# Kernel tuning notes

Measured on AMD Instinct MI355X. Metric: run time of the kernel, lower is better.

The kernel has to match this reference:

```python
import jax, jax.numpy as jnp
import numpy as np

B, C, N, INPUT_DIM = 16, 19, 64, 200
VQ_DIM = 64
NUM_EMBED = 8192
FREQ = INPUT_DIM // 2 + 1  # 101 rfft bins


def setup_inputs() -> dict:
    key = jax.random.key(0)
    k_x, k_pa, k_pp, k_ca, k_cp = jax.random.split(key, 5)
    x = jax.random.normal(k_x, (B, C, N, INPUT_DIM), dtype=jnp.float32)
    # xavier_normal for [FREQ, VQ_DIM]
    std = float(np.sqrt(2.0 / (FREQ + VQ_DIM)))
    proj_amp = jax.random.normal(k_pa, (FREQ, VQ_DIM), dtype=jnp.float32) * std
    proj_phase = jax.random.normal(k_pp, (FREQ, VQ_DIM), dtype=jnp.float32) * std
    codebook_amp = jax.random.uniform(k_ca, (NUM_EMBED, VQ_DIM), dtype=jnp.float32)
    codebook_phase = jax.random.uniform(k_cp, (NUM_EMBED, VQ_DIM), dtype=jnp.float32)
    return {"x": x, "proj_amp": proj_amp, "proj_phase": proj_phase,
            "codebook_amp": codebook_amp, "codebook_phase": codebook_phase}


def _l2norm(v):
    return v / jnp.linalg.norm(v, axis=-1, keepdims=True)


def reference(x, proj_amp, proj_phase, codebook_amp, codebook_phase):
    # rfft over last dim with ortho norm -> [B,C,N,FREQ] complex
    x_fft = jnp.fft.rfft(x, axis=-1, norm="ortho")
    amp = jnp.abs(x_fft)
    phase = jnp.angle(x_fft)
    # project to vq space and L2-normalize features and codebooks
    feat_amp = _l2norm(amp @ proj_amp)        # [B,C,N,D]
    feat_phase = _l2norm(phase @ proj_phase)  # [B,C,N,D]
    cb_amp = _l2norm(codebook_amp)            # [M,D]
    cb_phase = _l2norm(codebook_phase)        # [M,D]
    # cosine similarity vs codebook, argmax over codebook axis
    sim_amp = jnp.einsum("bcnd,md->bcnm", feat_amp, cb_amp)
    sim_phase = jnp.einsum("bcnd,md->bcnm", feat_phase, cb_phase)
    idx_amp = jnp.argmax(sim_amp, axis=-1)
    idx_phase = jnp.argmax(sim_phase, axis=-1)
    return idx_amp, idx_phase
```

## Files before the change

### kernel.cpp

```cpp
#include <hip/hip_runtime.h>
#include <math.h>

constexpr int ROWS  = 19456;
constexpr int IN_DIM = 200;
constexpr int FREQ  = 101;
constexpr int VQD   = 64;
constexpr int NEMB  = 8192;
constexpr int DFT_BLOCKS = ROWS / 8;

typedef __attribute__((ext_vector_type(8))) short short8;
typedef __attribute__((ext_vector_type(4))) float floatx4;

__device__ __forceinline__ unsigned short f2bf(float v) {
    unsigned int u = __builtin_bit_cast(unsigned int, v);
    unsigned int r = u + 0x7fffu + ((u >> 16) & 1u);
    return (unsigned short)(r >> 16);
}
__device__ __forceinline__ float bf2f(unsigned short b) {
    unsigned int u = ((unsigned int)b) << 16;
    return __builtin_bit_cast(float, u);
}

__device__ __forceinline__ void cis_exact(int r, double& c, double& s) {
    if (r == 0)        { c =  1.0; s =  0.0; }
    else if (r == 50)  { c =  0.0; s = -1.0; }
    else if (r == 100) { c = -1.0; s =  0.0; }
    else if (r == 150) { c =  0.0; s =  1.0; }
    else {
        double ang = -6.283185307179586476925286766559 * (double)r / (double)IN_DIM;
        c = cos(ang); s = sin(ang);
    }
}

#define GLOAD_LDS(gp, lp) __builtin_amdgcn_global_load_lds( \
    (const __attribute__((address_space(1))) unsigned int*)(gp), \
    (__attribute__((address_space(3))) unsigned int*)(lp), 16, 0, 0)

constexpr size_t align256(size_t x) { return (x + 255) & ~(size_t)255; }
constexpr size_t SZ_FB    = (size_t)2 * ROWS * VQD * sizeof(unsigned short);
constexpr size_t OFF_FTH  = 0;
constexpr size_t OFF_FTL  = align256(OFF_FTH + SZ_FB);
constexpr size_t SZ_CBB   = (size_t)2 * NEMB * VQD * sizeof(unsigned short);
constexpr size_t OFF_CBH  = align256(OFF_FTL + SZ_FB);
constexpr size_t OFF_CBL  = align256(OFF_CBH + SZ_CBB);
constexpr size_t SZ_FD    = (size_t)2 * ROWS * VQD * sizeof(double);
constexpr size_t OFF_FD   = align256(OFF_CBL + SZ_CBB);
constexpr size_t SZ_INV   = (size_t)2 * NEMB * sizeof(double);
constexpr size_t OFF_INV  = align256(OFF_FD + SZ_FD);
constexpr size_t SZ_PI    = (size_t)2 * 4 * ROWS * sizeof(int);
constexpr size_t OFF_PI1  = align256(OFF_INV + SZ_INV);
constexpr size_t OFF_PI2  = align256(OFF_PI1 + SZ_PI);

__global__ __launch_bounds__(256) void dft_cb_kernel(
    const float* __restrict__ x, const float* __restrict__ projA, const float* __restrict__ projP,
    const float* __restrict__ cbA, const float* __restrict__ cbP,
    unsigned short* __restrict__ ftH, unsigned short* __restrict__ ftL, double* __restrict__ featD,
    unsigned short* __restrict__ cbH, unsigned short* __restrict__ cbL, double* __restrict__ invnD)
{
    __shared__ __align__(16) char smem[20064];
    const int tid = threadIdx.x;

    if (blockIdx.x >= DFT_BLOCKS) {
        float* tile = (float*)smem;
        float* inv  = (float*)(smem + 16640);
        const int bid2 = blockIdx.x - DFT_BLOCKS;
        const int which = bid2 >> 7;
        const int m0 = (bid2 & 127) * 64;
        const float* cb = which ? cbP : cbA;
        for (int e = tid; e < 4096; e += 256) {
            int c = e >> 6, d = e & 63;
            tile[c * 65 + d] = cb[(size_t)(m0 + c) * VQD + d];
        }
        __syncthreads();
        if (tid < 64) {
            double s = 0.0;
            for (int d2 = 0; d2 < 64; ++d2) { double v = (double)tile[tid * 65 + d2]; s += v * v; }
            inv[tid] = (float)(1.0 / sqrt(s));
            invnD[(size_t)which * NEMB + m0 + tid] = 1.0 / sqrt(s);
        }
        __syncthreads();
        for (int e = tid; e < 4096; e += 256) {
            int c = e >> 6, d = e & 63;
            float v = tile[c * 65 + d] * inv[c];
            unsigned short hb = f2bf(v);
            unsigned short lb = f2bf(v - bf2f(hb));
            size_t o = ((size_t)which * NEMB + m0 + c) * VQD + d;
            cbH[o] = hb; cbL[o] = lb;
        }
        return;
    }

    float* xsT  = (float*)smem;
    float* xpS  = (float*)(smem + 7200);
    float* xmS  = (float*)(smem + 10400);
    float* reS  = (float*)(smem + 13600);
    float* imS  = (float*)(smem + 16832);
    float* accS = (float*)(smem + 7200);
    const int r0 = blockIdx.x * 8;

    for (int e = tid; e < 8 * IN_DIM; e += 256) {
        int r = e / IN_DIM, n = e - r * IN_DIM;
        xsT[n * 9 + r] = x[(size_t)(r0 + r) * IN_DIM + n];
    }
    __syncthreads();

    for (int e = tid; e < 99 * 8; e += 256) {
        int n = (e >> 3) + 1, r = e & 7;
        float a = xsT[n * 9 + r];
        float b = xsT[(IN_DIM - n) * 9 + r];
        xpS[n * 8 + r] = a + b;
        xmS[n * 8 + r] = a - b;
    }
    __syncthreads();

    const int k = tid & 127, half = tid >> 7;
    float re[8], im[8];
    if (k < FREQ) {
        double c1, s1;
        cis_exact(k, c1, s1);
        const int n0 = half ? 51 : 1;
        double wc, ws;
        cis_exact((int)(((long long)k * n0) % IN_DIM), wc, ws);
#pragma unroll
        for (int r = 0; r < 8; ++r) { re[r] = 0.f; im[r] = 0.f; }
        if (half) {
            float sg = (k & 1) ? -1.f : 1.f;
#pragma unroll
            for (int r = 0; r < 8; ++r)
                re[r] = xsT[r] + sg * xsT[100 * 9 + r];
        }
        const int nEnd = half ? 100 : 51;
        for (int n = n0; n < nEnd; ++n) {
            const float* xpn = xpS + n * 8;
            const float* xmn = xmS + n * 8;
            float wcf = (float)wc, wsf = (float)ws;
#pragma unroll
            for (int r = 0; r < 8; ++r) {
                re[r] = fmaf(xpn[r], wcf, re[r]);
                im[r] = fmaf(xmn[r], wsf, im[r]);
            }
            double nwc = fma(wc, c1, -ws * s1);
            double nws = fma(wc, s1,  ws * c1);
            wc = nwc; ws = nws;
        }
        if (half) {
#pragma unroll
            for (int r = 0; r < 8; ++r) { reS[k * 8 + r] = re[r]; imS[k * 8 + r] = im[r]; }
        }
    }
    __syncthreads();
    if (half == 0 && k < FREQ) {
#pragma unroll
        for (int r = 0; r < 8; ++r) {
            re[r] += reS[k * 8 + r]; im[r] += imS[k * 8 + r];
            reS[k * 8 + r] = re[r];  imS[k * 8 + r] = im[r];
        }
    }
    __syncthreads();
    for (int e = tid; e < FREQ * 8; e += 256) {
        float c = reS[e], s = imS[e];
        float a2 = fmaf(c, c, s * s);
        float ampv, phv;
        if (a2 >= 0.04f) {
            ampv = sqrtf(a2);
            phv  = atan2f(s, c);
        } else {
            const int kk = e >> 3, rr = e & 7;
            double sg = (kk & 1) ? -1.0 : 1.0;
            double reD = (double)xsT[rr] + sg * (double)xsT[100 * 9 + rr];
            double imD = 0.0;
            double c1, s1;
            cis_exact(kk, c1, s1);
            double wc = c1, ws = s1;
            for (int n = 1; n < 100; ++n) {
                double a = (double)xsT[n * 9 + rr];
                double b = (double)xsT[(IN_DIM - n) * 9 + rr];
                reD = fma(a + b, wc, reD);
                imD = fma(a - b, ws, imD);
                double nwc = fma(wc, c1, -ws * s1);
                double nws = fma(wc, s1,  ws * c1);
                wc = nwc; ws = nws;
            }
            ampv = (float)sqrt(reD * reD + imD * imD);
            phv  = (float)atan2(imD, reD);
        }
        reS[e] = ampv; imS[e] = phv;
    }
    __syncthreads();

    const int d = tid & 63, which = (tid >> 6) & 1, grp = tid >> 7;
    const float* proj = which ? projP : projA;
    const float* srcF = which ? imS : reS;
    float acc[8];
#pragma unroll
    for (int r = 0; r < 8; ++r) acc[r] = 0.f;
    const int kkA = grp ? 51 : 0;
    const int kkB = grp ? FREQ : 51;
    for (int kk = kkA; kk < kkB; ++kk) {
        float p = proj[kk * VQD + d];
#pragma unroll
        for (int r = 0; r < 8; ++r) acc[r] = fmaf(srcF[kk * 8 + r], p, acc[r]);
    }
    if (grp) {
#pragma unroll
        for (int r = 0; r < 8; ++r) accS[(tid & 127) * 8 + r] = acc[r];
    }
    __syncthreads();
    if (grp == 0) {
#pragma unroll
        for (int r = 0; r < 8; ++r) acc[r] += accS[tid * 8 + r];
#pragma unroll
        for (int r = 0; r < 8; ++r) {
            size_t rowi = (size_t)which * ROWS + r0 + r;
            float vf = acc[r];
            unsigned short hb = f2bf(vf);
            unsigned short lb = f2bf(vf - bf2f(hb));
            ftH[rowi * VQD + d] = hb;
            ftL[rowi * VQD + d] = lb;
            featD[rowi * VQD + d] = (double)acc[r];
        }
    }
}

#define MFMA(a, b, c) __builtin_amdgcn_mfma_f32_16x16x32_bf16(a, b, c, 0, 0, 0)
#define UPD(val, s) do { float _v = (val); \
    bool _c1 = _v > b1v[s]; bool _c2 = _v > b2v[s]; \
    b2v[s] = _c1 ? b1v[s] : (_c2 ? _v : b2v[s]); \
    b2i[s] = _c1 ? b1i[s] : (_c2 ? idx : b2i[s]); \
    b1v[s] = _c1 ? _v : b1v[s]; \
    b1i[s] = _c1 ? idx : b1i[s]; } while (0)

__global__ __launch_bounds__(256, 3) void argmax_kernel(
    const unsigned short* __restrict__ ftH, const unsigned short* __restrict__ ftL,
    const unsigned short* __restrict__ cbH, const unsigned short* __restrict__ cbL,
    int* __restrict__ pi1, int* __restrict__ pi2)
{
    __shared__ __align__(16) char lds[33792];
    const int tid = threadIdx.x;
    const int f = blockIdx.y, z = blockIdx.z;
    const int r0 = blockIdx.x * 128;
    const int w = tid >> 6, lane = tid & 63;
    const int q = lane >> 4, cl = lane & 15;

    const unsigned short* ftHb = ftH + (size_t)f * ROWS * VQD;
    const unsigned short* ftLb = ftL + (size_t)f * ROWS * VQD;
    const unsigned short* cbHb = cbH + (size_t)f * NEMB * VQD;
    const unsigned short* cbLb = cbL + (size_t)f * NEMB * VQD;

    short8 aH00, aH01, aH10, aH11, aL00, aL01, aL10, aL11;
    {
        const size_t baseA = (size_t)(r0 + w * 32 + cl) * VQD + q * 8;
        const size_t baseB = baseA + (size_t)16 * VQD;
        aH00 = *(const short8*)(ftHb + baseA);
        aH01 = *(const short8*)(ftHb + baseA + 32);
        aH10 = *(const short8*)(ftHb + baseB);
        aH11 = *(const short8*)(ftHb + baseB + 32);
        aL00 = *(const short8*)(ftLb + baseA);
        aL01 = *(const short8*)(ftLb + baseA + 32);
        aL10 = *(const short8*)(ftLb + baseB);
        aL11 = *(const short8*)(ftLb + baseB + 32);
    }

    float b1v[8], b2v[8]; int b1i[8], b2i[8];
#pragma unroll
    for (int s = 0; s < 8; ++s) { b1v[s] = -INFINITY; b2v[s] = -INFINITY; b1i[s] = 0; b2i[s] = 0; }

    const int cBase = tid >> 3;
    const int jel   = (((tid & 7) ^ (cBase & 7)) << 3);
    const unsigned short* gH = cbHb + (size_t)(z * 2048 + cBase) * VQD + jel;
    const unsigned short* gL = cbLb + (size_t)(z * 2048 + cBase) * VQD + jel;

    const int p0 = ((q ^ (cl & 7)) << 4);
    const int p1 = p0 ^ 64;

#pragma unroll
    for (int r = 0; r < 2; ++r) {
        const size_t gofs = (size_t)(32 * r) * VQD;
        GLOAD_LDS(gH + gofs, lds + w * 1024 + r * 4096);
        GLOAD_LDS(gL + gofs, lds + 8192 + w * 1024 + r * 4096);
    }

    for (int it = 0; it < 32; ++it) {
        __syncthreads();
        if (it < 31) {
            char* nbuf = lds + ((it + 1) & 1) * 16384;
            const size_t gbase = (size_t)((it + 1) * 64) * VQD;
#pragma unroll
            for (int r = 0; r < 2; ++r) {
                const size_t gofs = gbase + (size_t)(32 * r) * VQD;
                GLOAD_LDS(gH + gofs, nbuf + w * 1024 + r * 4096);
                GLOAD_LDS(gL + gofs, nbuf + 8192 + w * 1024 + r * 4096);
            }
        }

        const char* buf = lds + (it & 1) * 16384;
        const int cbase = z * 2048 + it * 64;
#pragma unroll
        for (int nt = 0; nt < 4; ++nt) {
            const char* row = buf + (nt * 16 + cl) * 128;
            short8 bH0 = *(const short8*)(row + p0);
            short8 bH1 = *(const short8*)(row + p1);
            short8 bL0 = *(const short8*)(row + 8192 + p0);
            short8 bL1 = *(const short8*)(row + 8192 + p1);

            floatx4 acc0 = {0.f, 0.f, 0.f, 0.f};
            floatx4 acc1 = {0.f, 0.f, 0.f, 0.f};
            acc0 = MFMA(aH00, bH0, acc0);  acc1 = MFMA(aH10, bH0, acc1);
            acc0 = MFMA(aH01, bH1, acc0);  acc1 = MFMA(aH11, bH1, acc1);
            acc0 = MFMA(aH00, bL0, acc0);  acc1 = MFMA(aH10, bL0, acc1);
            acc0 = MFMA(aH01, bL1, acc0);  acc1 = MFMA(aH11, bL1, acc1);
            acc0 = MFMA(aL00, bH0, acc0);  acc1 = MFMA(aL10, bH0, acc1);
            acc0 = MFMA(aL01, bH1, acc0);  acc1 = MFMA(aL11, bH1, acc1);

            const int idx = cbase + nt * 16 + cl;
#pragma unroll
            for (int i = 0; i < 4; ++i) { UPD(acc0[i], i); UPD(acc1[i], 4 + i); }
        }
    }

    __syncthreads();
    float* redv = (float*)lds;
    int*   redi = (int*)(lds + 128 * 33 * 4);
#pragma unroll
    for (int s = 0; s < 8; ++s) {
        int rowl = w * 32 + ((s & 4) << 2) + q * 4 + (s & 3);
        int base = rowl * 33 + cl * 2;
        redv[base]     = b1v[s]; redi[base]     = b1i[s];
        redv[base + 1] = b2v[s]; redi[base + 1] = b2i[s];
    }
    __syncthreads();
    if (tid < 128) {
        float v1 = -INFINITY, v2 = -INFINITY; int i1 = 0x7fffffff, i2 = 0x7fffffff;
        for (int e = 0; e < 32; ++e) {
            float v = redv[tid * 33 + e]; int id = redi[tid * 33 + e];
            if (v > v1 || (v == v1 && id < i1)) { v2 = v1; i2 = i1; v1 = v; i1 = id; }
            else if (v > v2 || (v == v2 && id < i2)) { v2 = v; i2 = id; }
        }
        size_t p = ((size_t)(f * 4 + z)) * ROWS + r0 + tid;
        pi1[p] = i1; pi2[p] = i2;
    }
}

__global__ __launch_bounds__(256) void rescore_kernel(
    const double* __restrict__ featD, const double* __restrict__ invnD,
    const float* __restrict__ cbA, const float* __restrict__ cbP,
    const int* __restrict__ pi1, const int* __restrict__ pi2,
    int* __restrict__ out)
{
    const int tid = threadIdx.x;
    const int lane = tid & 63, wave = tid >> 6;
    const int task = blockIdx.x * 4 + wave;
    const int f = task / ROWS;
    const int row = task - f * ROWS;
    const float* cb = f ? cbP : cbA;
    const double fd = featD[((size_t)f * ROWS + row) * VQD + lane];

    int idxs[8];
#pragma unroll
    for (int c = 0; c < 8; ++c) {
        int zz = c >> 1;
        size_t p = ((size_t)(f * 4 + zz)) * ROWS + row;
        idxs[c] = (c & 1) ? pi2[p] : pi1[p];
    }
    double cv[8];
#pragma unroll
    for (int c = 0; c < 8; ++c)
        cv[c] = (double)cb[(size_t)idxs[c] * VQD + lane];

    double bestv = -1.0e300; int besti = 0x7fffffff;
#pragma unroll
    for (int c = 0; c < 8; ++c) {
        double t = fd * cv[c];
        for (int m = 32; m >= 1; m >>= 1) t += __shfl_xor(t, m, 64);
        double sim = t * invnD[(size_t)f * NEMB + idxs[c]];
        int idx = idxs[c];
        if (sim > bestv || (sim == bestv && idx < besti)) { bestv = sim; besti = idx; }
    }
    if (lane == 0) out[task] = besti;
}

extern "C" void kernel_launch(void* const* d_in, const int* in_sizes, int n_in,
                              void* d_out, int out_size, void* d_ws, size_t ws_size,
                              hipStream_t stream)
{
    const float* x     = (const float*)d_in[0];
    const float* projA = (const float*)d_in[1];
    const float* projP = (const float*)d_in[2];
    const float* cbA   = (const float*)d_in[3];
    const float* cbP   = (const float*)d_in[4];

    char* ws = (char*)d_ws;
    unsigned short* ftH   = (unsigned short*)(ws + OFF_FTH);
    unsigned short* ftL   = (unsigned short*)(ws + OFF_FTL);
    unsigned short* cbHp  = (unsigned short*)(ws + OFF_CBH);
    unsigned short* cbLp  = (unsigned short*)(ws + OFF_CBL);
    double*         featD = (double*)(ws + OFF_FD);
    double*         invnD = (double*)(ws + OFF_INV);
    int*            pi1   = (int*)(ws + OFF_PI1);
    int*            pi2   = (int*)(ws + OFF_PI2);

    dft_cb_kernel<<<DFT_BLOCKS + 256, 256, 0, stream>>>(
        x, projA, projP, cbA, cbP, ftH, ftL, featD, cbHp, cbLp, invnD);
    argmax_kernel<<<dim3(ROWS / 128, 2, 4), 256, 0, stream>>>(ftH, ftL, cbHp, cbLp, pi1, pi2);
    rescore_kernel<<<(2 * ROWS) / 4, 256, 0, stream>>>(featD, invnD, cbA, cbP, pi1, pi2, (int*)d_out);
}
```

Measured before the change: 306.1 us.

## Share twiddle table in LDS and parallelize rescore over candidates per lane group

The DFT stage now computes the exact cos/sin values once per block into a shared-memory table. The second half's start twiddle is derived from the first-frequency value by a quarter-turn rotation, which replaces two per-thread cis_exact calls. The rescore kernel splits each wave into eight 8-lane groups, one per candidate. Each lane does an 8-element partial dot product, and a shuffle-based argmax reduction follows, replacing eight sequential full-wave reductions. This reduces shuffle count and serial latency, at the cost of an extra barrier and reuse of the reS region for the table.

```diff
diff --git a/kernel.cpp b/kernel.cpp
--- a/kernel.cpp
+++ b/kernel.cpp
@@ -90,12 +90,13 @@
         return;
     }
 
-    float* xsT  = (float*)smem;
-    float* xpS  = (float*)(smem + 7200);
-    float* xmS  = (float*)(smem + 10400);
-    float* reS  = (float*)(smem + 13600);
-    float* imS  = (float*)(smem + 16832);
-    float* accS = (float*)(smem + 7200);
+    float*  xsT  = (float*)smem;
+    float*  xpS  = (float*)(smem + 7200);
+    float*  xmS  = (float*)(smem + 10400);
+    float*  reS  = (float*)(smem + 13600);
+    float*  imS  = (float*)(smem + 16832);
+    double* cisT = (double*)(smem + 13600);
+    float*  accS = (float*)(smem + 7200);
     const int r0 = blockIdx.x * 8;
 
     for (int e = tid; e < 8 * IN_DIM; e += 256) {
@@ -111,16 +112,33 @@
         xpS[n * 8 + r] = a + b;
         xmS[n * 8 + r] = a - b;
     }
+    if (tid < FREQ) {
+        double c, s;
+        cis_exact(tid, c, s);
+        cisT[tid * 2]     = c;
+        cisT[tid * 2 + 1] = s;
+    }
     __syncthreads();
 
     const int k = tid & 127, half = tid >> 7;
+    double c1 = 1.0, s1 = 0.0, wc = 1.0, ws = 0.0;
+    if (k < FREQ) {
+        c1 = cisT[k * 2]; s1 = cisT[k * 2 + 1];
+        if (!half) {
+            wc = c1; ws = s1;
+        } else {
+            switch (k & 3) {
+                case 0: wc =  c1; ws =  s1; break;
+                case 1: wc =  s1; ws = -c1; break;
+                case 2: wc = -c1; ws = -s1; break;
+                default: wc = -s1; ws =  c1; break;
+            }
+        }
+    }
+    __syncthreads();
+
     float re[8], im[8];
     if (k < FREQ) {
-        double c1, s1;
-        cis_exact(k, c1, s1);
-        const int n0 = half ? 51 : 1;
-        double wc, ws;
-        cis_exact((int)(((long long)k * n0) % IN_DIM), wc, ws);
 #pragma unroll
         for (int r = 0; r < 8; ++r) { re[r] = 0.f; im[r] = 0.f; }
         if (half) {
@@ -129,6 +147,7 @@
             for (int r = 0; r < 8; ++r)
                 re[r] = xsT[r] + sg * xsT[100 * 9 + r];
         }
+        const int n0   = half ? 51 : 1;
         const int nEnd = half ? 100 : 51;
         for (int n = n0; n < nEnd; ++n) {
             const float* xpn = xpS + n * 8;
@@ -169,17 +188,17 @@
             double sg = (kk & 1) ? -1.0 : 1.0;
             double reD = (double)xsT[rr] + sg * (double)xsT[100 * 9 + rr];
             double imD = 0.0;
-            double c1, s1;
-            cis_exact(kk, c1, s1);
-            double wc = c1, ws = s1;
+            double cc1, ss1;
+            cis_exact(kk, cc1, ss1);
+            double twc = cc1, tws = ss1;
             for (int n = 1; n < 100; ++n) {
                 double a = (double)xsT[n * 9 + rr];
                 double b = (double)xsT[(IN_DIM - n) * 9 + rr];
-                reD = fma(a + b, wc, reD);
-                imD = fma(a - b, ws, imD);
-                double nwc = fma(wc, c1, -ws * s1);
-                double nws = fma(wc, s1,  ws * c1);
-                wc = nwc; ws = nws;
+                reD = fma(a + b, twc, reD);
+                imD = fma(a - b, tws, imD);
+                double nwc = fma(twc, cc1, -tws * ss1);
+                double nws = fma(twc, ss1,  tws * cc1);
+                twc = nwc; tws = nws;
             }
             ampv = (float)sqrt(reD * reD + imD * imD);
             phv  = (float)atan2(imD, reD);
@@ -353,30 +372,31 @@
     const int f = task / ROWS;
     const int row = task - f * ROWS;
     const float* cb = f ? cbP : cbA;
-    const double fd = featD[((size_t)f * ROWS + row) * VQD + lane];
-
-    int idxs[8];
-#pragma unroll
-    for (int c = 0; c < 8; ++c) {
-        int zz = c >> 1;
-        size_t p = ((size_t)(f * 4 + zz)) * ROWS + row;
-        idxs[c] = (c & 1) ? pi2[p] : pi1[p];
-    }
-    double cv[8];
-#pragma unroll
-    for (int c = 0; c < 8; ++c)
-        cv[c] = (double)cb[(size_t)idxs[c] * VQD + lane];
-
-    double bestv = -1.0e300; int besti = 0x7fffffff;
-#pragma unroll
-    for (int c = 0; c < 8; ++c) {
-        double t = fd * cv[c];
-        for (int m = 32; m >= 1; m >>= 1) t += __shfl_xor(t, m, 64);
-        double sim = t * invnD[(size_t)f * NEMB + idxs[c]];
-        int idx = idxs[c];
-        if (sim > bestv || (sim == bestv && idx < besti)) { bestv = sim; besti = idx; }
-    }
-    if (lane == 0) out[task] = besti;
+
+    const int c  = lane >> 3;
+    const int dp = (lane & 7) * 8;
+
+    const int zz = c >> 1;
+    const size_t p = ((size_t)(f * 4 + zz)) * ROWS + row;
+    const int idx = (c & 1) ? pi2[p] : pi1[p];
+
+    const double* fr = featD + ((size_t)f * ROWS + row) * VQD + dp;
+    const float*  cr = cb + (size_t)idx * VQD + dp;
+    double t = 0.0;
+#pragma unroll
+    for (int j = 0; j < 8; ++j) t = fma(fr[j], (double)cr[j], t);
+    t += __shfl_xor(t, 1, 64);
+    t += __shfl_xor(t, 2, 64);
+    t += __shfl_xor(t, 4, 64);
+    double bv = t * invnD[(size_t)f * NEMB + idx];
+    int    bi = idx;
+#pragma unroll
+    for (int m = 8; m <= 32; m <<= 1) {
+        double ov = __shfl_xor(bv, m, 64);
+        int    oi = __shfl_xor(bi, m, 64);
+        if (ov > bv || (ov == bv && oi < bi)) { bv = ov; bi = oi; }
+    }
+    if (lane == 0) out[task] = bi;
 }
 
 extern "C" void kernel_launch(void* const* d_in, const int* in_sizes, int n_in,
```

Measured after the change: 276.1 us. 1.11x faster.
